# Optimization experiments

Hardware: AMD Instinct MI355X
Metric: run time of the kernel (lower is better)

## Reference

```python
import jax, jax.numpy as jnp
import numpy as np

B, S, H, E = 4, 2048, 1024, 8


def setup_inputs() -> dict:
    key = jax.random.key(0)
    k1, k2, k3 = jax.random.split(key, 3)
    scale = 1.0 / np.sqrt(H)
    return {
        "x": jax.random.normal(k1, (B, S, H), dtype=jnp.float32),
        "router_w": jax.random.normal(k2, (H, E), dtype=jnp.float32) * scale,
        "router_b": jnp.zeros((E,), dtype=jnp.float32),
        "expert_w": jax.random.normal(k3, (E, H, H), dtype=jnp.float32) * scale,
        "expert_b": jnp.zeros((E, H), dtype=jnp.float32),
    }


def reference(x, router_w, router_b, expert_w, expert_b):
    # Flatten tokens: [T, H]
    b, s, h = x.shape
    hs = x.reshape(-1, h)
    # Router: logits -> softmax -> top-1 expert (argmax), matching the
    # original forward which routes each token to argmax(softmax(logits)).
    logits = hs @ router_w + router_b                 # [T, E]
    probs = jax.nn.softmax(logits, axis=-1)           # [T, E]
    idx = jnp.argmax(probs, axis=-1)                  # [T]
    gate = jnp.take_along_axis(probs, idx[:, None], axis=-1)  # [T, 1]
    # Per-expert GEMM computed densely for all experts (reference baseline
    # for the sort/dispatch + grouped-GEMM kernel): [T, E, H]
    expert_out = jnp.einsum("th,ehd->ted", hs, expert_w) + expert_b
    # Combine: select routed expert's output, weight by gate value.
    dispatch = jax.nn.one_hot(idx, expert_w.shape[0], dtype=hs.dtype) * gate  # [T, E]
    out = jnp.einsum("te,ted->td", dispatch, expert_out)  # [T, H]
    return out.reshape(b, s, h)
```

## Files before the change

kernel.cpp:

```cpp
#include <hip/hip_runtime.h>

constexpr int kT = 8192;
constexpr int kH = 1024;
constexpr int kE = 8;
constexpr int kMaxTiles = 72;
constexpr int kCntStride = 32;

typedef short short8 __attribute__((ext_vector_type(8)));
typedef float floatx4 __attribute__((ext_vector_type(4)));

__device__ inline unsigned short f2b(float f) {
    union { float f; unsigned int u; } v; v.f = f;
    unsigned int r = v.u + 0x7FFFu + ((v.u >> 16) & 1u);
    return (unsigned short)(r >> 16);
}

#define GLDS16(gp, lp)                                                                  \
    __builtin_amdgcn_global_load_lds(                                                   \
        (const __attribute__((address_space(1))) unsigned int*)(gp),                    \
        (__attribute__((address_space(3))) unsigned int*)(lp), 16, 0, 0)

__global__ __launch_bounds__(256) void k_prep(const float* __restrict__ W,
                                              unsigned short* __restrict__ Wt,
                                              const float* __restrict__ x,
                                              unsigned short* __restrict__ xb,
                                              const float* __restrict__ rw,
                                              const float* __restrict__ rb,
                                              float* __restrict__ gate,
                                              int* __restrict__ idx,
                                              int* __restrict__ cnt,
                                              int* __restrict__ done) {
    __shared__ __align__(16) char smem[32768];
    int bid = blockIdx.x;
    int tid = threadIdx.x;
    if (bid == 0 && tid < kE + 1) {
        if (tid < kE) cnt[tid * kCntStride] = 0; else *done = 0;
    }
    if (bid < 2048) {
        float (*lds)[65] = (float(*)[65])smem;
        int kb = bid & 15, nb = (bid >> 4) & 15, e = bid >> 8;
        int rr = tid >> 4, c4 = tid & 15;
        const float* Wp = W + ((size_t)e << 20) + (size_t)(kb * 64) * kH + nb * 64;
#pragma unroll
        for (int p = 0; p < 4; ++p) {
            int r = p * 16 + rr;
            float4 v = *(const float4*)(Wp + (size_t)r * kH + c4 * 4);
            lds[r][c4 * 4 + 0] = v.x; lds[r][c4 * 4 + 1] = v.y;
            lds[r][c4 * 4 + 2] = v.z; lds[r][c4 * 4 + 3] = v.w;
        }
        __syncthreads();
        unsigned short* Wo = Wt + ((size_t)e << 20) + (size_t)(nb * 64) * kH + kb * 64;
#pragma unroll
        for (int p = 0; p < 4; ++p) {
            int n = p * 16 + rr;
            ushort4 o;
            o.x = f2b(lds[c4 * 4 + 0][n]);
            o.y = f2b(lds[c4 * 4 + 1][n]);
            o.z = f2b(lds[c4 * 4 + 2][n]);
            o.w = f2b(lds[c4 * 4 + 3][n]);
            *(ushort4*)(Wo + (size_t)n * kH + c4 * 4) = o;
        }
        return;
    }
    float* rwlds = (float*)smem;
    int rbk = bid - 2048;
    int w = tid >> 6, lane = tid & 63;
#pragma unroll
    for (int i = 0; i < 8; ++i) {
        int g = i * 256 + tid;
        float4 v = *(const float4*)(rw + 4 * g);
        int pq = g ^ ((g >> 3) & 7);
        *(float4*)&rwlds[4 * pq] = v;
    }
    __syncthreads();
    for (int tk = 0; tk < 2; ++tk) {
        int t = rbk * 8 + w * 2 + tk;
        const float* xp = x + (size_t)t * kH;
        unsigned short* xop = xb + (size_t)t * kH;
        float pe[8];
#pragma unroll
        for (int e2 = 0; e2 < 8; ++e2) pe[e2] = 0.f;
#pragma unroll
        for (int j = 0; j < 4; ++j) {
            int h0 = j * 256 + lane * 4;
            float4 xv = *(const float4*)(xp + h0);
            ushort4 o;
            o.x = f2b(xv.x); o.y = f2b(xv.y); o.z = f2b(xv.z); o.w = f2b(xv.w);
            *(ushort4*)(xop + h0) = o;
            float xa[4] = {xv.x, xv.y, xv.z, xv.w};
#pragma unroll
            for (int c = 0; c < 4; ++c) {
                int q0 = 2 * (h0 + c);
                int key = (q0 >> 3) & 7;
                float4 w0 = *(const float4*)&rwlds[4 * (q0 ^ key)];
                float4 w1 = *(const float4*)&rwlds[4 * ((q0 + 1) ^ key)];
                float xs = xa[c];
                pe[0] += xs * w0.x; pe[1] += xs * w0.y;
                pe[2] += xs * w0.z; pe[3] += xs * w0.w;
                pe[4] += xs * w1.x; pe[5] += xs * w1.y;
                pe[6] += xs * w1.z; pe[7] += xs * w1.w;
            }
        }
#pragma unroll
        for (int s = 1; s < 64; s <<= 1)
#pragma unroll
            for (int e2 = 0; e2 < 8; ++e2) pe[e2] += __shfl_xor(pe[e2], s);
        if (lane == 0) {
            float m = pe[0] + rb[0]; int bi = 0;
#pragma unroll
            for (int e2 = 1; e2 < 8; ++e2) {
                float l = pe[e2] + rb[e2];
                if (l > m) { m = l; bi = e2; }
            }
            float sum = 0.f;
#pragma unroll
            for (int e2 = 0; e2 < 8; ++e2) sum += __expf(pe[e2] + rb[e2] - m);
            gate[t] = 1.0f / sum;
            idx[t]  = bi;
        }
    }
}

__global__ __launch_bounds__(256) void k_rank(const int* __restrict__ idx,
                                              int* __restrict__ perm2,
                                              int* __restrict__ cnt,
                                              int* __restrict__ done,
                                              int* __restrict__ tile_e,
                                              int* __restrict__ tile_row) {
    __shared__ int lcnt[kE];
    __shared__ int lbase[kE];
    int tid = threadIdx.x;
    if (tid < kE) lcnt[tid] = 0;
    __syncthreads();
    int t = blockIdx.x * 256 + tid;
    int bi = idx[t];
    int lrank = atomicAdd(&lcnt[bi], 1);
    __syncthreads();
    if (tid < kE) lbase[tid] = atomicAdd(&cnt[tid * kCntStride], lcnt[tid]);
    __syncthreads();
    perm2[bi * kT + lbase[bi] + lrank] = t;
    __syncthreads();
    if (tid == 0) {
        __threadfence();
        int old = atomicAdd(done, 1);
        if (old == (int)gridDim.x - 1) {
            __threadfence();
            int tt = 0;
            for (int ee = 0; ee < kE; ++ee) {
                int c = atomicAdd(&cnt[ee * kCntStride], 0);
                int nt = (c + 127) >> 7;
                for (int i = 0; i < nt; ++i) { tile_e[tt] = ee; tile_row[tt] = i << 7; ++tt; }
            }
            for (; tt < kMaxTiles; ++tt) tile_e[tt] = -1;
        }
    }
}

constexpr int kBK = 64;

__global__ __launch_bounds__(256, 3) void k_gemm(const unsigned short* __restrict__ xb,
                                                 const unsigned short* __restrict__ Wt,
                                                 const float* __restrict__ eb,
                                                 const int* __restrict__ perm2,
                                                 const float* __restrict__ gate,
                                                 const int* __restrict__ cnt,
                                                 const int* __restrict__ tile_e,
                                                 const int* __restrict__ tile_row,
                                                 float* __restrict__ out) {
    int bm = blockIdx.x, bn = blockIdx.y;
    int e = tile_e[bm];
    if (e < 0) return;
    int l0 = tile_row[bm];
    int ce = cnt[e * kCntStride];
    const int* pe = perm2 + e * kT;

    __shared__ __align__(16) unsigned short As[128 * kBK];
    __shared__ __align__(16) unsigned short Bs[128 * kBK];

    int tid = threadIdx.x;
    int wave = tid >> 6, lane = tid & 63;
    int wm = wave & 1, wn = wave >> 1;
    int quad = lane >> 4, l15 = lane & 15;

    floatx4 acc[4][4];
#pragma unroll
    for (int i = 0; i < 4; ++i)
#pragma unroll
        for (int j = 0; j < 4; ++j) acc[i][j] = floatx4{0.f, 0.f, 0.f, 0.f};

    int lrow8 = lane >> 3;
    int lseg8 = (lane & 7) ^ lrow8;
    const unsigned short* aPj[4];
#pragma unroll
    for (int j = 0; j < 4; ++j) {
        int lr = l0 + wave * 32 + j * 8 + lrow8;
        int tok = (lr < ce) ? pe[lr] : 0;
        aPj[j] = xb + (size_t)tok * kH + lseg8 * 8;
    }
    const unsigned short* bP = Wt + ((size_t)e << 20)
                             + (size_t)(bn * 128 + wave * 32 + lrow8) * kH + lseg8 * 8;
    unsigned short* lA = &As[(wave * 32) * kBK];
    unsigned short* lB = &Bs[(wave * 32) * kBK];

    for (int k0 = 0; k0 < kH; k0 += kBK) {
        __syncthreads();
#pragma unroll
        for (int j = 0; j < 4; ++j) {
            GLDS16(aPj[j] + k0, lA + j * 8 * kBK);
            GLDS16(bP + (size_t)(j * 8) * kH + k0, lB + j * 8 * kBK);
        }
        __syncthreads();

#pragma unroll
        for (int ks = 0; ks < 2; ++ks) {
            int sw = ((ks * 4 + quad) ^ (l15 & 7)) * 8;
            short8 af[4], bf[4];
#pragma unroll
            for (int i = 0; i < 4; ++i)
                af[i] = *(const short8*)&As[(wm * 64 + i * 16 + l15) * kBK + sw];
#pragma unroll
            for (int j = 0; j < 4; ++j)
                bf[j] = *(const short8*)&Bs[(wn * 64 + j * 16 + l15) * kBK + sw];
#pragma unroll
            for (int i = 0; i < 4; ++i)
#pragma unroll
                for (int j = 0; j < 4; ++j)
                    acc[i][j] = __builtin_amdgcn_mfma_f32_16x16x32_bf16(af[i], bf[j],
                                                                        acc[i][j], 0, 0, 0);
        }
    }

    int colbase = bn * 128 + wn * 64;
#pragma unroll
    for (int i = 0; i < 4; ++i) {
        int rl = l0 + wm * 64 + i * 16 + quad * 4;
#pragma unroll
        for (int rg = 0; rg < 4; ++rg) {
            int lr = rl + rg;
            if (lr >= ce) continue;
            int tok = pe[lr];
            float g = gate[tok];
            float* op = out + (size_t)tok * kH;
#pragma unroll
            for (int j = 0; j < 4; ++j) {
                int col = colbase + j * 16 + l15;
                op[col] = g * (acc[i][j][rg] + eb[e * kH + col]);
            }
        }
    }
}

extern "C" void kernel_launch(void* const* d_in, const int* in_sizes, int n_in,
                              void* d_out, int out_size, void* d_ws, size_t ws_size,
                              hipStream_t stream) {
    const float* x  = (const float*)d_in[0];
    const float* rw = (const float*)d_in[1];
    const float* rb = (const float*)d_in[2];
    const float* ew = (const float*)d_in[3];
    const float* eb = (const float*)d_in[4];
    float* out = (float*)d_out;

    char* p = (char*)d_ws;
    unsigned short* Wt = (unsigned short*)p; p += (size_t)kE * kH * kH * 2;
    unsigned short* xb = (unsigned short*)p; p += (size_t)kT * kH * 2;
    float* gate  = (float*)p; p += (size_t)kT * 4;
    int* idx     = (int*)p;   p += (size_t)kT * 4;
    int* perm2   = (int*)p;   p += (size_t)kE * kT * 4;
    int* cnt     = (int*)p;   p += kE * kCntStride * 4;
    int* done    = (int*)p;   p += 64;
    int* tile_e  = (int*)p;   p += kMaxTiles * 4;
    int* tile_r  = (int*)p;   p += kMaxTiles * 4;

    k_prep<<<3072, 256, 0, stream>>>(ew, Wt, x, xb, rw, rb, gate, idx, cnt, done);
    k_rank<<<kT / 256, 256, 0, stream>>>(idx, perm2, cnt, done, tile_e, tile_r);
    dim3 gg(kMaxTiles, kH / 128);
    k_gemm<<<gg, 256, 0, stream>>>(xb, Wt, eb, perm2, gate, cnt, tile_e, tile_r, out);
}
```

Measured before the change: 158.4 us.

## Split prep into transpose and router kernels with bf16 LDS transpose

Splits the fused prep kernel into a dedicated weight-transpose kernel and a separate router kernel. The transpose now converts to bf16 before staging in LDS, uses larger 64x128 tiles with an XOR swizzle, and writes 16-byte vectors instead of 8-byte ones. The router kernel processes 4 tokens per wave instead of 2, so it launches fewer blocks. The aim is to cut LDS traffic and bank conflicts and to widen global stores, at the cost of an extra kernel launch and losing overlap between the two prep jobs.

```diff
diff --git a/kernel.cpp b/kernel.cpp
--- a/kernel.cpp
+++ b/kernel.cpp
@@ -20,51 +20,49 @@
         (const __attribute__((address_space(1))) unsigned int*)(gp),                    \
         (__attribute__((address_space(3))) unsigned int*)(lp), 16, 0, 0)
 
-__global__ __launch_bounds__(256) void k_prep(const float* __restrict__ W,
-                                              unsigned short* __restrict__ Wt,
-                                              const float* __restrict__ x,
-                                              unsigned short* __restrict__ xb,
-                                              const float* __restrict__ rw,
-                                              const float* __restrict__ rb,
-                                              float* __restrict__ gate,
-                                              int* __restrict__ idx,
-                                              int* __restrict__ cnt,
-                                              int* __restrict__ done) {
-    __shared__ __align__(16) char smem[32768];
-    int bid = blockIdx.x;
-    int tid = threadIdx.x;
+__global__ __launch_bounds__(256) void k_trans(const float* __restrict__ W,
+                                               unsigned short* __restrict__ Wt,
+                                               int* __restrict__ cnt,
+                                               int* __restrict__ done) {
+    __shared__ __align__(16) unsigned short lt[64][136];
+    int bid = blockIdx.x, tid = threadIdx.x;
     if (bid == 0 && tid < kE + 1) {
         if (tid < kE) cnt[tid * kCntStride] = 0; else *done = 0;
     }
-    if (bid < 2048) {
-        float (*lds)[65] = (float(*)[65])smem;
-        int kb = bid & 15, nb = (bid >> 4) & 15, e = bid >> 8;
-        int rr = tid >> 4, c4 = tid & 15;
-        const float* Wp = W + ((size_t)e << 20) + (size_t)(kb * 64) * kH + nb * 64;
-#pragma unroll
-        for (int p = 0; p < 4; ++p) {
-            int r = p * 16 + rr;
-            float4 v = *(const float4*)(Wp + (size_t)r * kH + c4 * 4);
-            lds[r][c4 * 4 + 0] = v.x; lds[r][c4 * 4 + 1] = v.y;
-            lds[r][c4 * 4 + 2] = v.z; lds[r][c4 * 4 + 3] = v.w;
-        }
-        __syncthreads();
-        unsigned short* Wo = Wt + ((size_t)e << 20) + (size_t)(nb * 64) * kH + kb * 64;
-#pragma unroll
-        for (int p = 0; p < 4; ++p) {
-            int n = p * 16 + rr;
-            ushort4 o;
-            o.x = f2b(lds[c4 * 4 + 0][n]);
-            o.y = f2b(lds[c4 * 4 + 1][n]);
-            o.z = f2b(lds[c4 * 4 + 2][n]);
-            o.w = f2b(lds[c4 * 4 + 3][n]);
-            *(ushort4*)(Wo + (size_t)n * kH + c4 * 4) = o;
-        }
-        return;
-    }
-    float* rwlds = (float*)smem;
-    int rbk = bid - 2048;
-    int w = tid >> 6, lane = tid & 63;
+    int e = bid >> 7, kb = (bid >> 3) & 15, nb2 = bid & 7;
+    const float* Wp = W + ((size_t)e << 20) + (size_t)(kb * 64) * kH + nb2 * 128;
+    int c = (tid & 31) * 4;
+#pragma unroll
+    for (int i = 0; i < 8; ++i) {
+        int r = i * 8 + (tid >> 5);
+        float4 v = *(const float4*)(Wp + (size_t)r * kH + c);
+        int cp = c ^ (4 * ((r >> 3) & 7));
+        ushort4 o;
+        o.x = f2b(v.x); o.y = f2b(v.y); o.z = f2b(v.z); o.w = f2b(v.w);
+        *(ushort4*)&lt[r][cp] = o;
+    }
+    __syncthreads();
+    int k4 = (tid & 7) * 8;
+    unsigned short* Wo = Wt + ((size_t)e << 20) + (size_t)(nb2 * 128) * kH + kb * 64 + k4;
+#pragma unroll
+    for (int p = 0; p < 4; ++p) {
+        int n = p * 32 + (tid >> 3);
+        int cp = n ^ (4 * (tid & 7));
+        union { unsigned short u[8]; short8 s; } pk;
+#pragma unroll
+        for (int i = 0; i < 8; ++i) pk.u[i] = lt[k4 + i][cp];
+        *(short8*)(Wo + (size_t)n * kH) = pk.s;
+    }
+}
+
+__global__ __launch_bounds__(256) void k_router(const float* __restrict__ x,
+                                                unsigned short* __restrict__ xb,
+                                                const float* __restrict__ rw,
+                                                const float* __restrict__ rb,
+                                                float* __restrict__ gate,
+                                                int* __restrict__ idx) {
+    __shared__ __align__(16) float rwlds[8192];
+    int bid = blockIdx.x, tid = threadIdx.x;
 #pragma unroll
     for (int i = 0; i < 8; ++i) {
         int g = i * 256 + tid;
@@ -73,8 +71,9 @@
         *(float4*)&rwlds[4 * pq] = v;
     }
     __syncthreads();
-    for (int tk = 0; tk < 2; ++tk) {
-        int t = rbk * 8 + w * 2 + tk;
+    int w = tid >> 6, lane = tid & 63;
+    for (int tk = 0; tk < 4; ++tk) {
+        int t = bid * 16 + w * 4 + tk;
         const float* xp = x + (size_t)t * kH;
         unsigned short* xop = xb + (size_t)t * kH;
         float pe[8];
@@ -89,12 +88,12 @@
             *(ushort4*)(xop + h0) = o;
             float xa[4] = {xv.x, xv.y, xv.z, xv.w};
 #pragma unroll
-            for (int c = 0; c < 4; ++c) {
-                int q0 = 2 * (h0 + c);
+            for (int cc = 0; cc < 4; ++cc) {
+                int q0 = 2 * (h0 + cc);
                 int key = (q0 >> 3) & 7;
                 float4 w0 = *(const float4*)&rwlds[4 * (q0 ^ key)];
                 float4 w1 = *(const float4*)&rwlds[4 * ((q0 + 1) ^ key)];
-                float xs = xa[c];
+                float xs = xa[cc];
                 pe[0] += xs * w0.x; pe[1] += xs * w0.y;
                 pe[2] += xs * w0.z; pe[3] += xs * w0.w;
                 pe[4] += xs * w1.x; pe[5] += xs * w1.y;
@@ -271,7 +270,8 @@
     int* tile_e  = (int*)p;   p += kMaxTiles * 4;
     int* tile_r  = (int*)p;   p += kMaxTiles * 4;
 
-    k_prep<<<3072, 256, 0, stream>>>(ew, Wt, x, xb, rw, rb, gate, idx, cnt, done);
+    k_trans<<<1024, 256, 0, stream>>>(ew, Wt, cnt, done);
+    k_router<<<512, 256, 0, stream>>>(x, xb, rw, rb, gate, idx);
     k_rank<<<kT / 256, 256, 0, stream>>>(idx, perm2, cnt, done, tile_e, tile_r);
     dim3 gg(kMaxTiles, kH / 128);
     k_gemm<<<gg, 256, 0, stream>>>(xb, Wt, eb, perm2, gate, cnt, tile_e, tile_r, out);
```

Result: no change. 160.3 us (+1.2%).
